# Performance work log

Hardware: AMD Instinct MI355X
Metric: run time of the kernel (lower is better)

The kernel has to match this reference:

```python
import jax, jax.numpy as jnp
import numpy as np

N = 1_000_000   # number of groups (== number of atoms here)
D = 128         # in_dim
B = 4096        # B_sub (number of graphs)
STEPS = 2       # processing_steps


def setup_inputs() -> dict:
    key = jax.random.key(0)
    k1, k2, k3, k4, k5, k6 = jax.random.split(key, 6)
    s = 1.0 / np.sqrt(D)  # torch LSTM init bound
    xg_local = jax.random.normal(k1, (N, D), dtype=jnp.float32)
    # a2g_local[0]=group idx, a2g_local[1]=atom idx; identity map covers all groups
    a2g_local = jnp.stack([jnp.arange(N), jnp.arange(N)]).astype(jnp.int32)
    batch_sub = jnp.sort(jax.random.randint(k2, (N,), 0, B)).astype(jnp.int32)
    # LSTM(input=2D, hidden=D, num_layers=1) params, torch gate order i,f,g,o
    W_ih = jax.random.uniform(k3, (4 * D, 2 * D), jnp.float32, -s, s)
    W_hh = jax.random.uniform(k4, (4 * D, D), jnp.float32, -s, s)
    b_ih = jax.random.uniform(k5, (4 * D,), jnp.float32, -s, s)
    b_hh = jax.random.uniform(k6, (4 * D,), jnp.float32, -s, s)
    return dict(xg_local=xg_local, a2g_local=a2g_local, batch_sub=batch_sub,
                W_ih=W_ih, W_hh=W_hh, b_ih=b_ih, b_hh=b_hh)


def _set2set(x, batch, present, W_ih, W_hh, b_ih, b_hh):
    # Set2Set pooling: iterative LSTM + segment-softmax attention + scatter-add.
    h = jnp.zeros((B, D), x.dtype)
    c = jnp.zeros((B, D), x.dtype)
    q_star = jnp.zeros((B, 2 * D), x.dtype)
    for _ in range(STEPS):
        gates = q_star @ W_ih.T + b_ih + h @ W_hh.T + b_hh  # [B, 4D]
        i, f, g, o = jnp.split(gates, 4, axis=-1)
        c = jax.nn.sigmoid(f) * c + jax.nn.sigmoid(i) * jnp.tanh(g)
        h = jax.nn.sigmoid(o) * jnp.tanh(c)
        q = h                                                # [B, D]
        e = jnp.sum(x * q[batch], axis=-1)                   # [N]
        e_max = jax.ops.segment_max(e, batch, num_segments=B)
        e_max = jnp.where(present, e_max, 0.0)               # guard empty segments
        ex = jnp.exp(e - e_max[batch])
        denom = jax.ops.segment_sum(ex, batch, num_segments=B)
        a = ex / jnp.where(present, denom, 1.0)[batch]       # segment softmax
        r = jax.ops.segment_sum(a[:, None] * x, batch, num_segments=B)  # [B, D]
        q_star = jnp.concatenate([q, r], axis=-1)
    return q_star


def reference(xg_local, a2g_local, batch_sub, W_ih, W_hh, b_ih, b_hh):
    batch_sub = batch_sub.astype(jnp.int32)
    # group -> batch assignment via scatter
    gb = jnp.full((N,), -1, dtype=jnp.int32)
    gb = gb.at[a2g_local[0]].set(batch_sub[a2g_local[1]])
    # unassigned groups get the mode of batch_sub
    default_b = jnp.argmax(jnp.bincount(batch_sub, length=B)).astype(jnp.int32)
    gb = jnp.where(gb < 0, default_b, gb)
    counts = jax.ops.segment_sum(jnp.ones((N,), jnp.float32), gb, num_segments=B)
    present = counts > 0  # [B] which samples have at least one group
    q_star = _set2set(xg_local, gb, present, W_ih, W_hh, b_ih, b_hh)
    # samples with no groups -> zero rows (out[present] = out_compact semantics)
    return jnp.where(present[:, None], q_star, 0.0)
```

## Files before the change

kernel.cpp:

```cpp
#include <hip/hip_runtime.h>
#include <math.h>


#define D 128

static __device__ __forceinline__ float sigf(float x) { return 1.0f / (1.0f + expf(-x)); }


__global__ void k_scatter(const int* __restrict__ a2g, const int* __restrict__ bs,
                          int* __restrict__ gb, int n) {
    int k = blockIdx.x * 256 + threadIdx.x;
    if (k < n) gb[a2g[k]] = bs[a2g[n + k]];
}

__global__ void k_bounds(const int* __restrict__ g, int n, int B, int* __restrict__ bnd) {
    int i = blockIdx.x * 256 + threadIdx.x;
    if (i >= n) return;
    int v = g[i];
    if (i == 0) {
        for (int b = 0; b <= v; ++b) bnd[b] = 0;
    } else {
        int p = g[i - 1];
        for (int b = p + 1; b <= v; ++b) bnd[b] = i;
    }
    if (i == n - 1) {
        for (int b = v + 1; b <= B; ++b) bnd[b] = n;
    }
}

__global__ void k_mode(const int* __restrict__ bnd, int B, int* __restrict__ dflt) {
    __shared__ int rc[256], ri[256];
    int t = threadIdx.x;
    int bc = -1, bi = 0;
    for (int b = t; b < B; b += 256) {
        int c = bnd[b + 1] - bnd[b];
        if (c > bc) { bc = c; bi = b; }
    }
    rc[t] = bc; ri[t] = bi;
    __syncthreads();
    for (int s = 128; s > 0; s >>= 1) {
        if (t < s) {
            if (rc[t + s] > rc[t] || (rc[t + s] == rc[t] && ri[t + s] < ri[t])) {
                rc[t] = rc[t + s]; ri[t] = ri[t + s];
            }
        }
        __syncthreads();
    }
    if (t == 0) *dflt = ri[0];
}

__global__ void k_fill(int* __restrict__ gb, const int* __restrict__ dflt, int n) {
    int i = blockIdx.x * 256 + threadIdx.x;
    if (i < n && gb[i] < 0) gb[i] = *dflt;
}

__global__ void k_gates0(const float* __restrict__ bih, const float* __restrict__ bhh,
                         float* __restrict__ h1, float* __restrict__ c1) {
    int d = threadIdx.x;
    float gi = bih[d] + bhh[d];
    float gg = bih[2 * D + d] + bhh[2 * D + d];
    float go = bih[3 * D + d] + bhh[3 * D + d];
    float c = sigf(gi) * tanhf(gg);
    c1[d] = c;
    h1[d] = sigf(go) * tanhf(c);
}

__global__ void k_gconst(const float* __restrict__ Wih, const float* __restrict__ Whh,
                         const float* __restrict__ bih, const float* __restrict__ bhh,
                         const float* __restrict__ h1, float* __restrict__ gc) {
    int j = blockIdx.x * 256 + threadIdx.x;
    float s = bih[j] + bhh[j];
    for (int d = 0; d < D; ++d) s += h1[d] * (Wih[(size_t)j * 2 * D + d] + Whh[(size_t)j * D + d]);
    gc[j] = s;
}

__global__ __launch_bounds__(256) void k_attn(const float* __restrict__ x,
                                              const float* __restrict__ qsrc, int qstride,
                                              const int* __restrict__ seg,
                                              float* __restrict__ r) {
    int b = blockIdx.x;
    int s0 = seg[b], s1 = seg[b + 1];
    int lane = threadIdx.x & 63, w = threadIdx.x >> 6;
    if (s0 >= s1) {
        if (threadIdx.x < 64) {
            r[(size_t)b * D + 2 * threadIdx.x] = 0.0f;
            r[(size_t)b * D + 2 * threadIdx.x + 1] = 0.0f;
        }
        return;
    }
    float2 qv = ((const float2*)(qsrc + (size_t)b * qstride))[lane];
    float m = -INFINITY, den = 0.0f, ax = 0.0f, ay = 0.0f;
    for (int n = s0 + w; n < s1; n += 4) {
        float2 xv = ((const float2*)(x + (size_t)n * D))[lane];
        float dot = fmaf(xv.x, qv.x, xv.y * qv.y);
#pragma unroll
        for (int off = 1; off < 64; off <<= 1) dot += __shfl_xor(dot, off, 64);
        if (dot > m) {
            float sc = expf(m - dot);
            den *= sc; ax *= sc; ay *= sc; m = dot;
        }
        float p = expf(dot - m);
        den += p;
        ax = fmaf(p, xv.x, ax);
        ay = fmaf(p, xv.y, ay);
    }
    __shared__ float sm[4], sd[4];
    __shared__ float sax[4][64], say[4][64];
    if (lane == 0) { sm[w] = m; sd[w] = den; }
    sax[w][lane] = ax; say[w][lane] = ay;
    __syncthreads();
    if (w == 0) {
        float M = fmaxf(fmaxf(sm[0], sm[1]), fmaxf(sm[2], sm[3]));
        float e0 = expf(sm[0] - M), e1 = expf(sm[1] - M);
        float e2 = expf(sm[2] - M), e3 = expf(sm[3] - M);
        float Dn = sd[0] * e0 + sd[1] * e1 + sd[2] * e2 + sd[3] * e3;
        float rx = sax[0][lane] * e0 + sax[1][lane] * e1 + sax[2][lane] * e2 + sax[3][lane] * e3;
        float ry = say[0][lane] * e0 + say[1][lane] * e1 + say[2][lane] * e2 + say[3][lane] * e3;
        float inv = 1.0f / Dn;
        float2 o; o.x = rx * inv; o.y = ry * inv;
        ((float2*)(r + (size_t)b * D))[lane] = o;
    }
}

#define TB 16
__global__ __launch_bounds__(256) void k_gemm(const float* __restrict__ r1,
                                              const float* __restrict__ Wih,
                                              const float* __restrict__ gc,
                                              float* __restrict__ gates) {
    __shared__ __align__(16) float At[TB * 132];
    int tid = threadIdx.x;
    int b0 = blockIdx.x * TB;
#pragma unroll
    for (int i = 0; i < 2; ++i) {
        int k = tid + i * 256;
        int row = k >> 5, c4 = k & 31;
        float4 v = ((const float4*)(r1 + (size_t)(b0 + row) * D))[c4];
        *((float4*)&At[row * 132 + c4 * 4]) = v;
    }
    __syncthreads();
    int j0 = tid, j1 = tid + 256;
    const float4* w0p = (const float4*)(Wih + (size_t)j0 * 2 * D + D);
    const float4* w1p = (const float4*)(Wih + (size_t)j1 * 2 * D + D);
    float acc0[TB], acc1[TB];
#pragma unroll
    for (int b = 0; b < TB; ++b) { acc0[b] = 0.0f; acc1[b] = 0.0f; }
    for (int k4 = 0; k4 < D / 4; ++k4) {
        float4 w0 = w0p[k4], w1 = w1p[k4];
#pragma unroll
        for (int b = 0; b < TB; ++b) {
            float4 a = *((const float4*)&At[b * 132 + k4 * 4]);
            acc0[b] = fmaf(a.x, w0.x, fmaf(a.y, w0.y, fmaf(a.z, w0.z, fmaf(a.w, w0.w, acc0[b]))));
            acc1[b] = fmaf(a.x, w1.x, fmaf(a.y, w1.y, fmaf(a.z, w1.z, fmaf(a.w, w1.w, acc1[b]))));
        }
    }
    float g0 = gc[j0], g1 = gc[j1];
    for (int b = 0; b < TB; ++b) {
        gates[(size_t)(b0 + b) * 512 + j0] = acc0[b] + g0;
        gates[(size_t)(b0 + b) * 512 + j1] = acc1[b] + g1;
    }
}

__global__ void k_lstm2(const float* __restrict__ gates, const float* __restrict__ c1,
                        float* __restrict__ h2) {
    int idx = blockIdx.x * 256 + threadIdx.x;
    int b = idx >> 7, d = idx & 127;
    const float* g = gates + (size_t)b * 512;
    float gi = g[d], gf = g[D + d], gg = g[2 * D + d], go = g[3 * D + d];
    float c = sigf(gf) * c1[d] + sigf(gi) * tanhf(gg);
    h2[idx] = sigf(go) * tanhf(c);
}

__global__ void k_out(const float* __restrict__ h2, const float* __restrict__ r2,
                      const int* __restrict__ seg, float* __restrict__ out) {
    int b = blockIdx.x, t = threadIdx.x;
    bool pres = seg[b + 1] > seg[b];
    float v = (t < D) ? h2[(size_t)b * D + t] : r2[(size_t)b * D + (t - D)];
    out[(size_t)b * 256 + t] = pres ? v : 0.0f;
}

extern "C" void kernel_launch(void* const* d_in, const int* in_sizes, int n_in,
                              void* d_out, int out_size, void* d_ws, size_t ws_size,
                              hipStream_t stream) {
    const float* x   = (const float*)d_in[0];
    const int*   a2g = (const int*)d_in[1];
    const int*   bs  = (const int*)d_in[2];
    const float* Wih = (const float*)d_in[3];
    const float* Whh = (const float*)d_in[4];
    const float* bih = (const float*)d_in[5];
    const float* bhh = (const float*)d_in[6];
    float* out = (float*)d_out;

    const int N = in_sizes[2];
    const int B = out_size / (2 * D);

    char* p = (char*)d_ws;
    auto alloc = [&](size_t bytes) { char* q = p; p += (bytes + 255) & ~(size_t)255; return q; };
    int*   gb    = (int*)alloc((size_t)N * 4);
    int*   bnd2  = (int*)alloc((size_t)(B + 1) * 4);
    int*   seg   = (int*)alloc((size_t)(B + 1) * 4);
    int*   dflt  = (int*)alloc(4);
    float* h1    = (float*)alloc(D * 4);
    float* c1    = (float*)alloc(D * 4);
    float* gc    = (float*)alloc(512 * 4);
    float* r1    = (float*)alloc((size_t)B * D * 4);
    float* gates = (float*)alloc((size_t)B * 512 * 4);
    float* h2    = (float*)alloc((size_t)B * D * 4);
    float* r2    = (float*)alloc((size_t)B * D * 4);

    int nb = (N + 255) / 256;
    hipMemsetAsync(gb, 0xFF, (size_t)N * 4, stream);
    k_scatter<<<nb, 256, 0, stream>>>(a2g, bs, gb, N);
    k_bounds<<<nb, 256, 0, stream>>>(bs, N, B, bnd2);
    k_mode<<<1, 256, 0, stream>>>(bnd2, B, dflt);
    k_fill<<<nb, 256, 0, stream>>>(gb, dflt, N);
    k_bounds<<<nb, 256, 0, stream>>>(gb, N, B, seg);

    k_gates0<<<1, D, 0, stream>>>(bih, bhh, h1, c1);
    k_attn<<<B, 256, 0, stream>>>(x, h1, 0, seg, r1);
    k_gconst<<<2, 256, 0, stream>>>(Wih, Whh, bih, bhh, h1, gc);
    k_gemm<<<B / TB, 256, 0, stream>>>(r1, Wih, gc, gates);
    k_lstm2<<<(B * D) / 256, 256, 0, stream>>>(gates, c1, h2);
    k_attn<<<B, 256, 0, stream>>>(x, h2, D, seg, r2);
    k_out<<<B, 256, 0, stream>>>(h2, r2, seg, out);
}
```

Measured before the change: 883.1 us.

## Process four rows per wavefront in attention and parallelize gate-constant dot products

The attention kernel now splits each wavefront into four 16-lane groups, each reading one row with two float4 loads. The dot product needs only a 4-step shuffle reduction, and the online softmax is updated per chunk of four rows, with a group-level reduction of the accumulators at the end. This cuts shuffle count per row and widens memory loads for the bandwidth-bound pass over x, at the cost of extra exp calls for the other groups' scores and clamped duplicate loads in tail chunks. Separately, the gate-constant kernel moves from 2 blocks of serial 128-step loops to 512 wavefronts, each doing a vectorized load and shuffle reduction.

After: 818.5 us. -7.3%, faster.

```diff
diff --git a/kernel.cpp b/kernel.cpp
--- a/kernel.cpp
+++ b/kernel.cpp
@@ -65,13 +65,20 @@
     h1[d] = sigf(go) * tanhf(c);
 }
 
-__global__ void k_gconst(const float* __restrict__ Wih, const float* __restrict__ Whh,
-                         const float* __restrict__ bih, const float* __restrict__ bhh,
-                         const float* __restrict__ h1, float* __restrict__ gc) {
-    int j = blockIdx.x * 256 + threadIdx.x;
-    float s = bih[j] + bhh[j];
-    for (int d = 0; d < D; ++d) s += h1[d] * (Wih[(size_t)j * 2 * D + d] + Whh[(size_t)j * D + d]);
-    gc[j] = s;
+__global__ __launch_bounds__(64) void k_gconst(const float* __restrict__ Wih,
+                                               const float* __restrict__ Whh,
+                                               const float* __restrict__ bih,
+                                               const float* __restrict__ bhh,
+                                               const float* __restrict__ h1,
+                                               float* __restrict__ gc) {
+    int j = blockIdx.x, lane = threadIdx.x;
+    float2 wa = ((const float2*)(Wih + (size_t)j * 2 * D))[lane];
+    float2 wb = ((const float2*)(Whh + (size_t)j * D))[lane];
+    float2 h  = ((const float2*)h1)[lane];
+    float s = h.x * (wa.x + wb.x) + h.y * (wa.y + wb.y);
+#pragma unroll
+    for (int off = 1; off < 64; off <<= 1) s += __shfl_xor(s, off, 64);
+    if (lane == 0) gc[j] = s + bih[j] + bhh[j];
 }
 
 __global__ __launch_bounds__(256) void k_attn(const float* __restrict__ x,
@@ -80,44 +87,73 @@
                                               float* __restrict__ r) {
     int b = blockIdx.x;
     int s0 = seg[b], s1 = seg[b + 1];
-    int lane = threadIdx.x & 63, w = threadIdx.x >> 6;
+    int tid = threadIdx.x;
     if (s0 >= s1) {
-        if (threadIdx.x < 64) {
-            r[(size_t)b * D + 2 * threadIdx.x] = 0.0f;
-            r[(size_t)b * D + 2 * threadIdx.x + 1] = 0.0f;
+        if (tid < 64) ((float2*)(r + (size_t)b * D))[tid] = make_float2(0.f, 0.f);
+        return;
+    }
+    int lane = tid & 63, w = tid >> 6;
+    int g = lane >> 4;
+    int c0 = (lane & 15) * 8;
+    const float* qp = qsrc + (size_t)b * qstride + c0;
+    float4 q0 = *(const float4*)(qp);
+    float4 q1 = *(const float4*)(qp + 4);
+    float m = -INFINITY, den = 0.0f;
+    float4 a0 = make_float4(0.f, 0.f, 0.f, 0.f);
+    float4 a1 = make_float4(0.f, 0.f, 0.f, 0.f);
+    for (int n = s0 + w * 4; n < s1; n += 16) {
+        int row = n + g;
+        int rc = row < s1 ? row : s1 - 1;
+        const float* xp = x + (size_t)rc * D + c0;
+        float4 v0 = *(const float4*)(xp);
+        float4 v1 = *(const float4*)(xp + 4);
+        float d = fmaf(v0.x, q0.x, fmaf(v0.y, q0.y, fmaf(v0.z, q0.z, v0.w * q0.w)))
+                + fmaf(v1.x, q1.x, fmaf(v1.y, q1.y, fmaf(v1.z, q1.z, v1.w * q1.w)));
+        d += __shfl_xor(d, 1, 64);
+        d += __shfl_xor(d, 2, 64);
+        d += __shfl_xor(d, 4, 64);
+        d += __shfl_xor(d, 8, 64);
+        if (row >= s1) d = -INFINITY;
+        float o1 = __shfl_xor(d, 16, 64);
+        float o2 = __shfl_xor(d, 32, 64);
+        float o3 = __shfl_xor(o1, 32, 64);
+        float cmax = fmaxf(fmaxf(d, o1), fmaxf(o2, o3));
+        if (cmax > m) {
+            float sc = expf(m - cmax);
+            den *= sc;
+            a0.x *= sc; a0.y *= sc; a0.z *= sc; a0.w *= sc;
+            a1.x *= sc; a1.y *= sc; a1.z *= sc; a1.w *= sc;
+            m = cmax;
         }
-        return;
-    }
-    float2 qv = ((const float2*)(qsrc + (size_t)b * qstride))[lane];
-    float m = -INFINITY, den = 0.0f, ax = 0.0f, ay = 0.0f;
-    for (int n = s0 + w; n < s1; n += 4) {
-        float2 xv = ((const float2*)(x + (size_t)n * D))[lane];
-        float dot = fmaf(xv.x, qv.x, xv.y * qv.y);
-#pragma unroll
-        for (int off = 1; off < 64; off <<= 1) dot += __shfl_xor(dot, off, 64);
-        if (dot > m) {
-            float sc = expf(m - dot);
-            den *= sc; ax *= sc; ay *= sc; m = dot;
-        }
-        float p = expf(dot - m);
-        den += p;
-        ax = fmaf(p, xv.x, ax);
-        ay = fmaf(p, xv.y, ay);
-    }
-    __shared__ float sm[4], sd[4];
-    __shared__ float sax[4][64], say[4][64];
-    if (lane == 0) { sm[w] = m; sd[w] = den; }
-    sax[w][lane] = ax; say[w][lane] = ay;
+        float p = expf(d - m);
+        den += p + expf(o1 - m) + expf(o2 - m) + expf(o3 - m);
+        a0.x = fmaf(p, v0.x, a0.x); a0.y = fmaf(p, v0.y, a0.y);
+        a0.z = fmaf(p, v0.z, a0.z); a0.w = fmaf(p, v0.w, a0.w);
+        a1.x = fmaf(p, v1.x, a1.x); a1.y = fmaf(p, v1.y, a1.y);
+        a1.z = fmaf(p, v1.z, a1.z); a1.w = fmaf(p, v1.w, a1.w);
+    }
+#define GRED(F) F += __shfl_xor(F, 16, 64); F += __shfl_xor(F, 32, 64);
+    GRED(a0.x) GRED(a0.y) GRED(a0.z) GRED(a0.w)
+    GRED(a1.x) GRED(a1.y) GRED(a1.z) GRED(a1.w)
+#undef GRED
+    __shared__ float sm[4], sden[4];
+    __shared__ __align__(16) float sacc[4][D];
+    if (lane == 0) { sm[w] = m; sden[w] = den; }
+    if (lane < 16) {
+        ((float4*)&sacc[w][c0])[0] = a0;
+        ((float4*)&sacc[w][c0])[1] = a1;
+    }
     __syncthreads();
     if (w == 0) {
         float M = fmaxf(fmaxf(sm[0], sm[1]), fmaxf(sm[2], sm[3]));
         float e0 = expf(sm[0] - M), e1 = expf(sm[1] - M);
         float e2 = expf(sm[2] - M), e3 = expf(sm[3] - M);
-        float Dn = sd[0] * e0 + sd[1] * e1 + sd[2] * e2 + sd[3] * e3;
-        float rx = sax[0][lane] * e0 + sax[1][lane] * e1 + sax[2][lane] * e2 + sax[3][lane] * e3;
-        float ry = say[0][lane] * e0 + say[1][lane] * e1 + say[2][lane] * e2 + say[3][lane] * e3;
+        float Dn = e0 * sden[0] + e1 * sden[1] + e2 * sden[2] + e3 * sden[3];
         float inv = 1.0f / Dn;
-        float2 o; o.x = rx * inv; o.y = ry * inv;
+        int c = 2 * lane;
+        float2 o;
+        o.x = (e0 * sacc[0][c] + e1 * sacc[1][c] + e2 * sacc[2][c] + e3 * sacc[3][c]) * inv;
+        o.y = (e0 * sacc[0][c + 1] + e1 * sacc[1][c + 1] + e2 * sacc[2][c + 1] + e3 * sacc[3][c + 1]) * inv;
         ((float2*)(r + (size_t)b * D))[lane] = o;
     }
 }
@@ -217,7 +253,7 @@
 
     k_gates0<<<1, D, 0, stream>>>(bih, bhh, h1, c1);
     k_attn<<<B, 256, 0, stream>>>(x, h1, 0, seg, r1);
-    k_gconst<<<2, 256, 0, stream>>>(Wih, Whh, bih, bhh, h1, gc);
+    k_gconst<<<512, 64, 0, stream>>>(Wih, Whh, bih, bhh, h1, gc);
     k_gemm<<<B / TB, 256, 0, stream>>>(r1, Wih, gc, gates);
     k_lstm2<<<(B * D) / 256, 256, 0, stream>>>(gates, c1, h2);
     k_attn<<<B, 256, 0, stream>>>(x, h2, D, seg, r2);
```
